# Performance work log

Measured on AMD Instinct MI355X. Metric: run time of the kernel, lower is better.

The kernel has to match this reference:

```python
import jax, jax.numpy as jnp
import numpy as np

N_USERS = 100000
N_ITEMS = 200000
N_NODES = N_USERS + N_ITEMS
EMB = 64
N_HOPS = 3
NNZ = 2000000
EDGE_RATE = 0.5   # edge_dropout_rate
MESS_RATE = 0.1   # mess_dropout_rate


def setup_inputs() -> dict:
    key = jax.random.key(0)
    k1, k2, k3, k4, k5 = jax.random.split(key, 5)
    user_embed = jax.random.normal(k1, (N_USERS, EMB), dtype=jnp.float32) * 0.1
    item_embed = jax.random.normal(k2, (N_ITEMS, EMB), dtype=jnp.float32) * 0.1
    adj_rows = jax.random.randint(k3, (NNZ,), 0, N_NODES, dtype=jnp.int32)
    adj_cols = jax.random.randint(k4, (NNZ,), 0, N_NODES, dtype=jnp.int32)
    # normalized adjacency values (positive, small) like D^-1/2 A D^-1/2 entries
    adj_vals = jax.random.uniform(k5, (NNZ,), dtype=jnp.float32) * 0.1
    return {
        "user_embed": user_embed,
        "item_embed": item_embed,
        "adj_vals": adj_vals,
        "adj_rows": adj_rows,
        "adj_cols": adj_cols,
    }


def reference(user_embed, item_embed, adj_vals, adj_rows, adj_cols):
    # all_embed: [N_NODES, EMB]
    agg = jnp.concatenate([user_embed, item_embed], axis=0)
    drop_key = jax.random.key(42)
    embs = []
    for hop in range(N_HOPS):
        ekey = jax.random.fold_in(drop_key, 2 * hop)
        mkey = jax.random.fold_in(drop_key, 2 * hop + 1)
        # sparse edge dropout: mask = floor(rate + U[0,1)) -> keep w.p. rate,
        # rescale kept values by 1/(1-rate), exactly as _sparse_dropout
        edge_keep = jnp.floor(EDGE_RATE + jax.random.uniform(ekey, (NNZ,))) > 0
        v = jnp.where(edge_keep, adj_vals, 0.0) * (1.0 / (1.0 - EDGE_RATE))
        # SpMM: out[r] += v_e * agg[c] for each edge e=(r,c)
        msgs = v[:, None] * agg[adj_cols]                 # [NNZ, EMB]
        agg = jax.ops.segment_sum(msgs, adj_rows, num_segments=N_NODES)
        # message dropout (nn.Dropout): keep w.p. 1-p, scale 1/(1-p)
        keep = jax.random.uniform(mkey, agg.shape) >= MESS_RATE
        agg = jnp.where(keep, agg, 0.0) * (1.0 / (1.0 - MESS_RATE))
        embs.append(agg)
    embs = jnp.stack(embs, axis=1)  # [N_NODES, N_HOPS, EMB]
    # original returns (embs[:n_users], embs[n_users:]); we return the
    # concatenated stack (identical math, split is a view)
    return embs
```

## Files before the change

kernel.cpp:

```cpp
#include <hip/hip_runtime.h>
#include <cstdint>

static constexpr int kUsers  = 100000;
static constexpr int kItems  = 200000;
static constexpr int kNodes  = 300000;
static constexpr int kEmb    = 64;
static constexpr int kHops   = 3;
static constexpr int kNnz    = 2000000;
static constexpr int kStride = kHops * kEmb;

#define MESS_SCALE ((float)(1.0 / 0.9))

__host__ __device__ inline void tf2x32(uint32_t k0, uint32_t k1, uint32_t& x0, uint32_t& x1) {
  uint32_t k2 = k0 ^ k1 ^ 0x1BD11BDAu;
  x0 += k0; x1 += k1;
#define TFR(r) { x0 += x1; x1 = (x1 << (r)) | (x1 >> (32 - (r))); x1 ^= x0; }
  TFR(13) TFR(15) TFR(26) TFR(6)
  x0 += k1; x1 += k2 + 1u;
  TFR(17) TFR(29) TFR(16) TFR(24)
  x0 += k2; x1 += k0 + 2u;
  TFR(13) TFR(15) TFR(26) TFR(6)
  x0 += k0; x1 += k1 + 3u;
  TFR(17) TFR(29) TFR(16) TFR(24)
  x0 += k1; x1 += k2 + 4u;
  TFR(13) TFR(15) TFR(26) TFR(6)
  x0 += k2; x1 += k0 + 5u;
#undef TFR
}

__device__ inline uint32_t draw_bits(uint32_t k0, uint32_t k1, uint32_t i) {
  uint32_t x0 = 0u, x1 = i;
  tf2x32(k0, k1, x0, x1);
  return x0 ^ x1;
}

__device__ inline float bits_to_unit(uint32_t bits) {
  return __uint_as_float((bits >> 9) | 0x3F800000u) - 1.0f;
}


__global__ void hist_k(const int* __restrict__ rows, int* __restrict__ deg) {
  int e = blockIdx.x * blockDim.x + threadIdx.x;
  if (e < kNnz) atomicAdd(&deg[rows[e]], 1);
}

__global__ void alloc_k(const int* __restrict__ deg, int* __restrict__ start,
                        int* __restrict__ cur, int* __restrict__ cursor) {
  int r = blockIdx.x * blockDim.x + threadIdx.x;
  int lane = threadIdx.x & 63;
  int d = (r < kNodes) ? deg[r] : 0;
  int x = d;
  for (int off = 1; off < 64; off <<= 1) {
    int y = __shfl_up(x, off);
    if (lane >= off) x += y;
  }
  int excl = x - d;
  int total = __shfl(x, 63);
  int base = 0;
  if (lane == 63) base = atomicAdd(cursor, total);
  base = __shfl(base, 63);
  if (r < kNodes) { start[r] = base + excl; cur[r] = base + excl; }
}

__global__ void fill_k(const int* __restrict__ rows, const int* __restrict__ cols,
                       const float* __restrict__ vals, int* __restrict__ cur,
                       int* __restrict__ cols_s, float* __restrict__ vals_s,
                       int* __restrict__ eid_s) {
  int e = blockIdx.x * blockDim.x + threadIdx.x;
  if (e >= kNnz) return;
  int r = rows[e];
  int p = atomicAdd(&cur[r], 1);
  cols_s[p] = cols[e];
  vals_s[p] = vals[e];
  eid_s[p]  = e;
}


__global__ void edge_vals_csr_k(const int* __restrict__ eid_s, const float* __restrict__ vals_s,
                                float* __restrict__ vbuf, uint32_t ek0, uint32_t ek1) {
  int p = blockIdx.x * blockDim.x + threadIdx.x;
  if (p >= kNnz) return;
  uint32_t bits = draw_bits(ek0, ek1, (uint32_t)eid_s[p]);
  vbuf[p] = (bits & 0x80000000u) ? vals_s[p] * 2.0f : 0.0f;
}

__global__ void row_gather_k(const int* __restrict__ start, const int* __restrict__ deg,
                             const int* __restrict__ cols_s, const float* __restrict__ vbuf,
                             const float* __restrict__ user_emb, const float* __restrict__ item_emb,
                             const float* __restrict__ prev,
                             float* __restrict__ out, uint32_t mk0, uint32_t mk1, int hop) {
  int wid = (int)(((long long)blockIdx.x * blockDim.x + threadIdx.x) >> 6);
  int d = threadIdx.x & 63;
  if (wid >= kNodes) return;
  int s = start[wid];
  int n = deg[wid];
  float acc = 0.0f;
  float v = 0.0f; int c = 0;
  if (n > 0) { v = vbuf[s]; c = cols_s[s]; }
  for (int k = 0; k < n; ++k) {
    float vn = 0.0f; int cn = 0;
    if (k + 1 < n) { vn = vbuf[s + k + 1]; cn = cols_s[s + k + 1]; }
    if (v != 0.0f) {
      float x;
      if (prev) {
        x = prev[(long long)c * kStride + d];
      } else {
        x = (c < kUsers) ? user_emb[(long long)c * kEmb + d]
                         : item_emb[(long long)(c - kUsers) * kEmb + d];
      }
      acc += v * x;
    }
    v = vn; c = cn;
  }
  uint32_t bits = draw_bits(mk0, mk1, (uint32_t)(wid * kEmb + d));
  float u = bits_to_unit(bits);
  float res = (u >= 0.1f) ? acc * MESS_SCALE : 0.0f;
  out[(long long)wid * kStride + hop * kEmb + d] = res;
}


__global__ void edge_vals_k(const float* __restrict__ adj_vals, float* __restrict__ v_out,
                            uint32_t ek0, uint32_t ek1) {
  int e = blockIdx.x * blockDim.x + threadIdx.x;
  if (e >= kNnz) return;
  uint32_t bits = draw_bits(ek0, ek1, (uint32_t)e);
  v_out[e] = (bits & 0x80000000u) ? adj_vals[e] * 2.0f : 0.0f;
}

__global__ void scatter_k(const int* __restrict__ rows, const int* __restrict__ cols,
                          const float* __restrict__ vvals,
                          const float* __restrict__ user_emb, const float* __restrict__ item_emb,
                          const float* __restrict__ prev, float* __restrict__ acc) {
  long long t = (long long)blockIdx.x * blockDim.x + threadIdx.x;
  int e = (int)(t >> 6);
  int d = (int)(t & 63);
  if (e >= kNnz) return;
  float ve = vvals[e];
  if (ve == 0.0f) return;
  int c = cols[e];
  int r = rows[e];
  float x;
  if (prev) x = prev[(long long)c * kStride + d];
  else x = (c < kUsers) ? user_emb[(long long)c * kEmb + d]
                        : item_emb[(long long)(c - kUsers) * kEmb + d];
  unsafeAtomicAdd(&acc[(long long)r * kStride + d], ve * x);
}

__global__ void mess_k(float* __restrict__ slice, uint32_t mk0, uint32_t mk1) {
  long long i = (long long)blockIdx.x * blockDim.x + threadIdx.x;
  const long long total = (long long)kNodes * kEmb;
  if (i >= total) return;
  uint32_t bits = draw_bits(mk0, mk1, (uint32_t)i);
  float u = bits_to_unit(bits);
  int n = (int)(i >> 6), d = (int)(i & 63);
  long long idx = (long long)n * kStride + d;
  float val = slice[idx];
  slice[idx] = (u >= 0.1f) ? val * MESS_SCALE : 0.0f;
}


extern "C" void kernel_launch(void* const* d_in, const int* in_sizes, int n_in,
                              void* d_out, int out_size, void* d_ws, size_t ws_size,
                              hipStream_t stream) {
  const float* user_emb = (const float*)d_in[0];
  const float* item_emb = (const float*)d_in[1];
  const float* adj_vals = (const float*)d_in[2];
  const int*   adj_rows = (const int*)d_in[3];
  const int*   adj_cols = (const int*)d_in[4];
  float* out = (float*)d_out;

  char* base = (char*)d_ws;
  const size_t off_deg    = 0;
  const size_t off_start  = 1200128;
  const size_t off_cur    = 2400256;
  const size_t off_cursor = 3600384;
  const size_t off_cols   = 3600896;
  const size_t off_vals   = 11600896;
  const size_t off_eid    = 19600896;
  const size_t off_vbuf   = 27600896;
  const size_t needed     = 35600896;

  uint32_t ek0[kHops], ek1[kHops], mk0[kHops], mk1[kHops];
  for (int hop = 0; hop < kHops; ++hop) {
    ek0[hop] = 0u; ek1[hop] = (uint32_t)(2 * hop);
    tf2x32(0u, 42u, ek0[hop], ek1[hop]);
    mk0[hop] = 0u; mk1[hop] = (uint32_t)(2 * hop + 1);
    tf2x32(0u, 42u, mk0[hop], mk1[hop]);
  }

  if (ws_size >= needed) {
    int*   deg    = (int*)(base + off_deg);
    int*   start  = (int*)(base + off_start);
    int*   cur    = (int*)(base + off_cur);
    int*   cursor = (int*)(base + off_cursor);
    int*   cols_s = (int*)(base + off_cols);
    float* vals_s = (float*)(base + off_vals);
    int*   eid_s  = (int*)(base + off_eid);
    float* vbuf   = (float*)(base + off_vbuf);

    hipMemsetAsync(deg, 0, (size_t)kNodes * sizeof(int), stream);
    hipMemsetAsync(cursor, 0, sizeof(int), stream);

    hist_k<<<(kNnz + 255) / 256, 256, 0, stream>>>(adj_rows, deg);
    alloc_k<<<(kNodes + 255) / 256, 256, 0, stream>>>(deg, start, cur, cursor);
    fill_k<<<(kNnz + 255) / 256, 256, 0, stream>>>(adj_rows, adj_cols, adj_vals,
                                                   cur, cols_s, vals_s, eid_s);

    for (int hop = 0; hop < kHops; ++hop) {
      edge_vals_csr_k<<<(kNnz + 255) / 256, 256, 0, stream>>>(eid_s, vals_s, vbuf,
                                                              ek0[hop], ek1[hop]);
      const float* prev = (hop == 0) ? nullptr : (out + (long long)(hop - 1) * kEmb);
      long long nthreads = (long long)kNodes * 64;
      row_gather_k<<<(int)((nthreads + 255) / 256), 256, 0, stream>>>(
          start, deg, cols_s, vbuf, user_emb, item_emb, prev, out,
          mk0[hop], mk1[hop], hop);
    }
  } else {
    float* vbuf = (float*)d_ws;
    hipMemsetAsync(d_out, 0, (size_t)out_size * sizeof(float), stream);
    for (int hop = 0; hop < kHops; ++hop) {
      edge_vals_k<<<(kNnz + 255) / 256, 256, 0, stream>>>(adj_vals, vbuf, ek0[hop], ek1[hop]);
      const float* prev = (hop == 0) ? nullptr : (out + (long long)(hop - 1) * kEmb);
      float* acc = out + (long long)hop * kEmb;
      long long nthreads = (long long)kNnz * 64;
      scatter_k<<<(int)((nthreads + 255) / 256), 256, 0, stream>>>(
          adj_rows, adj_cols, vbuf, user_emb, item_emb, prev, acc);
      long long etotal = (long long)kNodes * kEmb;
      mess_k<<<(int)((etotal + 255) / 256), 256, 0, stream>>>(acc, mk0[hop], mk1[hop]);
    }
  }
}
```

Measured before the change: 1.172 ms.

## Pack CSR edge data into int4 records and unroll row gather by four

Replaces the separate cols/vals/eid/vbuf arrays with one interleaved int4 record per edge (col, eid, val, dropped value), so each gather step does one 16-byte load instead of two scattered loads. The row gather loop is unrolled by four with clamped indices so four embedding loads are in flight at once, and it uses the post-fill cursor array as the row end pointer. Hop 0 and later hops become separate template instantiations, which removes the per-edge prev branch. The zero-value skip is gone, so dropped edges now still fetch their embedding row, which adds memory traffic in exchange for branch-free, higher memory-level parallelism.

Result: faster. 974.2 us (-16.9%).

```diff
diff --git a/kernel.cpp b/kernel.cpp
--- a/kernel.cpp
+++ b/kernel.cpp
@@ -64,53 +64,63 @@
 
 __global__ void fill_k(const int* __restrict__ rows, const int* __restrict__ cols,
                        const float* __restrict__ vals, int* __restrict__ cur,
-                       int* __restrict__ cols_s, float* __restrict__ vals_s,
-                       int* __restrict__ eid_s) {
+                       int4* __restrict__ pv) {
   int e = blockIdx.x * blockDim.x + threadIdx.x;
   if (e >= kNnz) return;
   int r = rows[e];
   int p = atomicAdd(&cur[r], 1);
-  cols_s[p] = cols[e];
-  vals_s[p] = vals[e];
-  eid_s[p]  = e;
-}
-
-
-__global__ void edge_vals_csr_k(const int* __restrict__ eid_s, const float* __restrict__ vals_s,
-                                float* __restrict__ vbuf, uint32_t ek0, uint32_t ek1) {
+  pv[p] = make_int4(cols[e], e, __float_as_int(vals[e]), 0);
+}
+
+
+__global__ void edge_vals_csr_k(int4* __restrict__ pv, uint32_t ek0, uint32_t ek1) {
   int p = blockIdx.x * blockDim.x + threadIdx.x;
   if (p >= kNnz) return;
-  uint32_t bits = draw_bits(ek0, ek1, (uint32_t)eid_s[p]);
-  vbuf[p] = (bits & 0x80000000u) ? vals_s[p] * 2.0f : 0.0f;
-}
-
-__global__ void row_gather_k(const int* __restrict__ start, const int* __restrict__ deg,
-                             const int* __restrict__ cols_s, const float* __restrict__ vbuf,
-                             const float* __restrict__ user_emb, const float* __restrict__ item_emb,
+  int4 ee = pv[p];
+  uint32_t bits = draw_bits(ek0, ek1, (uint32_t)ee.y);
+  float v = (bits & 0x80000000u) ? __int_as_float(ee.z) * 2.0f : 0.0f;
+  ((int*)pv)[4 * p + 3] = __float_as_int(v);
+}
+
+template <bool HOP0>
+__global__ void row_gather_k(const int* __restrict__ start, const int* __restrict__ endp,
+                             const int4* __restrict__ pv,
+                             const float* __restrict__ ue, const float* __restrict__ ie,
                              const float* __restrict__ prev,
                              float* __restrict__ out, uint32_t mk0, uint32_t mk1, int hop) {
   int wid = (int)(((long long)blockIdx.x * blockDim.x + threadIdx.x) >> 6);
   int d = threadIdx.x & 63;
   if (wid >= kNodes) return;
-  int s = start[wid];
-  int n = deg[wid];
+  int s = endp ? start[wid] : 0;
+  int e = endp[wid];
   float acc = 0.0f;
-  float v = 0.0f; int c = 0;
-  if (n > 0) { v = vbuf[s]; c = cols_s[s]; }
-  for (int k = 0; k < n; ++k) {
-    float vn = 0.0f; int cn = 0;
-    if (k + 1 < n) { vn = vbuf[s + k + 1]; cn = cols_s[s + k + 1]; }
-    if (v != 0.0f) {
-      float x;
-      if (prev) {
-        x = prev[(long long)c * kStride + d];
-      } else {
-        x = (c < kUsers) ? user_emb[(long long)c * kEmb + d]
-                         : item_emb[(long long)(c - kUsers) * kEmb + d];
-      }
-      acc += v * x;
+  const float* isft = ie - (long long)kUsers * kEmb;
+  for (int k = s; k < e; k += 4) {
+    int i1 = (k + 1 < e) ? k + 1 : e - 1;
+    int i2 = (k + 2 < e) ? k + 2 : e - 1;
+    int i3 = (k + 3 < e) ? k + 3 : e - 1;
+    int4 e0 = pv[k], e1 = pv[i1], e2 = pv[i2], e3 = pv[i3];
+    float v0 = __int_as_float(e0.w);
+    float v1 = (k + 1 < e) ? __int_as_float(e1.w) : 0.0f;
+    float v2 = (k + 2 < e) ? __int_as_float(e2.w) : 0.0f;
+    float v3 = (k + 3 < e) ? __int_as_float(e3.w) : 0.0f;
+    float x0, x1, x2, x3;
+    if (HOP0) {
+      const float* b0 = (e0.x < kUsers) ? ue : isft;
+      const float* b1 = (e1.x < kUsers) ? ue : isft;
+      const float* b2 = (e2.x < kUsers) ? ue : isft;
+      const float* b3 = (e3.x < kUsers) ? ue : isft;
+      x0 = b0[(long long)e0.x * kEmb + d];
+      x1 = b1[(long long)e1.x * kEmb + d];
+      x2 = b2[(long long)e2.x * kEmb + d];
+      x3 = b3[(long long)e3.x * kEmb + d];
+    } else {
+      x0 = prev[(long long)e0.x * kStride + d];
+      x1 = prev[(long long)e1.x * kStride + d];
+      x2 = prev[(long long)e2.x * kStride + d];
+      x3 = prev[(long long)e3.x * kStride + d];
     }
-    v = vn; c = cn;
+    acc += v0 * x0 + v1 * x1 + v2 * x2 + v3 * x3;
   }
   uint32_t bits = draw_bits(mk0, mk1, (uint32_t)(wid * kEmb + d));
   float u = bits_to_unit(bits);
@@ -174,10 +184,7 @@
   const size_t off_start  = 1200128;
   const size_t off_cur    = 2400256;
   const size_t off_cursor = 3600384;
-  const size_t off_cols   = 3600896;
-  const size_t off_vals   = 11600896;
-  const size_t off_eid    = 19600896;
-  const size_t off_vbuf   = 27600896;
+  const size_t off_pv     = 3600896;
   const size_t needed     = 35600896;
 
   uint32_t ek0[kHops], ek1[kHops], mk0[kHops], mk1[kHops];
@@ -189,31 +196,31 @@
   }
 
   if (ws_size >= needed) {
-    int*   deg    = (int*)(base + off_deg);
-    int*   start  = (int*)(base + off_start);
-    int*   cur    = (int*)(base + off_cur);
-    int*   cursor = (int*)(base + off_cursor);
-    int*   cols_s = (int*)(base + off_cols);
-    float* vals_s = (float*)(base + off_vals);
-    int*   eid_s  = (int*)(base + off_eid);
-    float* vbuf   = (float*)(base + off_vbuf);
+    int*  deg    = (int*)(base + off_deg);
+    int*  start  = (int*)(base + off_start);
+    int*  cur    = (int*)(base + off_cur);
+    int*  cursor = (int*)(base + off_cursor);
+    int4* pv     = (int4*)(base + off_pv);
 
     hipMemsetAsync(deg, 0, (size_t)kNodes * sizeof(int), stream);
     hipMemsetAsync(cursor, 0, sizeof(int), stream);
 
     hist_k<<<(kNnz + 255) / 256, 256, 0, stream>>>(adj_rows, deg);
     alloc_k<<<(kNodes + 255) / 256, 256, 0, stream>>>(deg, start, cur, cursor);
-    fill_k<<<(kNnz + 255) / 256, 256, 0, stream>>>(adj_rows, adj_cols, adj_vals,
-                                                   cur, cols_s, vals_s, eid_s);
-
+    fill_k<<<(kNnz + 255) / 256, 256, 0, stream>>>(adj_rows, adj_cols, adj_vals, cur, pv);
+
+    long long nthreads = (long long)kNodes * 64;
+    int ngrid = (int)((nthreads + 255) / 256);
     for (int hop = 0; hop < kHops; ++hop) {
-      edge_vals_csr_k<<<(kNnz + 255) / 256, 256, 0, stream>>>(eid_s, vals_s, vbuf,
-                                                              ek0[hop], ek1[hop]);
-      const float* prev = (hop == 0) ? nullptr : (out + (long long)(hop - 1) * kEmb);
-      long long nthreads = (long long)kNodes * 64;
-      row_gather_k<<<(int)((nthreads + 255) / 256), 256, 0, stream>>>(
-          start, deg, cols_s, vbuf, user_emb, item_emb, prev, out,
-          mk0[hop], mk1[hop], hop);
+      edge_vals_csr_k<<<(kNnz + 255) / 256, 256, 0, stream>>>(pv, ek0[hop], ek1[hop]);
+      if (hop == 0) {
+        row_gather_k<true><<<ngrid, 256, 0, stream>>>(
+            start, cur, pv, user_emb, item_emb, nullptr, out, mk0[hop], mk1[hop], hop);
+      } else {
+        const float* prev = out + (long long)(hop - 1) * kEmb;
+        row_gather_k<false><<<ngrid, 256, 0, stream>>>(
+            start, cur, pv, user_emb, item_emb, prev, out, mk0[hop], mk1[hop], hop);
+      }
     }
   } else {
     float* vbuf = (float*)d_ws;
```
